# Kernel tuning notes

Hardware: AMD Instinct MI355X
Metric: run time of the kernel (lower is better)

Reference implementation:

```python
import jax, jax.numpy as jnp
from jax import lax
import numpy as np

EPS = 1e-3  # keras BatchNormalization default epsilon

def _bn(x, g, b, m, v):
    return (x - m) / jnp.sqrt(v + EPS) * g + b

def _conv_relu(x, w, b):
    y = lax.conv_general_dilated(x, w, (1, 1), 'SAME', dimension_numbers=('NHWC', 'HWIO', 'NHWC'))
    return jax.nn.relu(y + b)

def _pool(x):
    return lax.reduce_window(x, -jnp.inf, lax.max, (1, 2, 2, 1), (1, 2, 2, 1), 'VALID')

def setup_inputs():
    key = jax.random.key(0)
    ks = jax.random.split(key, 24)
    B, E = 2048, 16
    rn = lambda k, s, sc=0.05: jax.random.normal(k, s, jnp.float32) * sc
    pos = lambda k, s: jax.random.uniform(k, s, jnp.float32, 0.5, 1.5)
    inp = {}
    inp['x'] = jax.random.normal(ks[0], (B, 32, 32, 3), jnp.float32)
    inp['cW1'] = rn(ks[1], (3, 3, 3, 32), 0.2); inp['cb1'] = jnp.zeros((32,), jnp.float32)
    inp['bn1g'] = pos(ks[2], (32,)); inp['bn1b'] = rn(ks[3], (32,))
    inp['bn1m'] = rn(ks[4], (32,)); inp['bn1v'] = pos(ks[5], (32,))
    inp['cW2'] = rn(ks[6], (3, 3, 32, 64), 0.1); inp['cb2'] = jnp.zeros((64,), jnp.float32)
    inp['bn2g'] = pos(ks[7], (64,)); inp['bn2b'] = rn(ks[8], (64,))
    inp['bn2m'] = rn(ks[9], (64,)); inp['bn2v'] = pos(ks[10], (64,))
    inp['dW'] = rn(ks[11], (4096, 128), 0.02); inp['db'] = jnp.zeros((128,), jnp.float32)
    inp['rW1'] = rn(ks[12], (128, 64), 0.1); inp['rb1'] = jnp.zeros((64,), jnp.float32)
    inp['rW2'] = rn(ks[13], (64, E), 0.1); inp['rb2'] = jnp.zeros((E,), jnp.float32)
    inp['eW1'] = rn(ks[14], (E, 128, 128), 0.1); inp['eb1'] = jnp.zeros((E, 128), jnp.float32)
    inp['ebng'] = pos(ks[15], (E, 128)); inp['ebnb'] = rn(ks[16], (E, 128))
    inp['ebnm'] = rn(ks[17], (E, 128)); inp['ebnv'] = pos(ks[18], (E, 128))
    inp['eW2'] = rn(ks[19], (E, 128, 64), 0.1); inp['eb2'] = jnp.zeros((E, 64), jnp.float32)
    inp['eW3'] = rn(ks[20], (E, 64, 10), 0.1); inp['eb3'] = jnp.zeros((E, 10), jnp.float32)
    return inp

def reference(x, cW1, cb1, bn1g, bn1b, bn1m, bn1v, cW2, cb2, bn2g, bn2b, bn2m, bn2v,
              dW, db, rW1, rb1, rW2, rb2, eW1, eb1, ebng, ebnb, ebnm, ebnv, eW2, eb2, eW3, eb3):
    # shared trunk: conv(relu) -> BN -> maxpool, twice; flatten; dense(relu). Dropout = identity (inference).
    h = _pool(_bn(_conv_relu(x, cW1, cb1), bn1g, bn1b, bn1m, bn1v))   # [B,16,16,32]
    h = _pool(_bn(_conv_relu(h, cW2, cb2), bn2g, bn2b, bn2m, bn2v))   # [B,8,8,64]
    feats = jax.nn.relu(h.reshape(h.shape[0], -1) @ dW + db)          # [B,128]
    # router softmax over expert logits
    router_logits = jax.nn.relu(feats @ rW1 + rb1) @ rW2 + rb2        # [B,E]
    router_probs = jax.nn.softmax(router_logits, axis=-1)
    # all experts fused into batched GEMMs over stacked weights: [E,B,*]
    e = jax.nn.relu(jnp.einsum('bd,edh->ebh', feats, eW1) + eb1[:, None, :])
    e = _bn(e, ebng[:, None, :], ebnb[:, None, :], ebnm[:, None, :], ebnv[:, None, :])
    e = jax.nn.relu(jnp.einsum('ebh,ehk->ebk', e, eW2) + eb2[:, None, :])
    e = jnp.einsum('ebk,ekc->ebc', e, eW3) + eb3[:, None, :]          # [E,B,10]
    # weighted sum combine: sum_e probs[b,e] * logits[e,b,c]
    return jnp.einsum('ebc,be->bc', e, router_probs)
```

## Files before the change

### kernel.cpp

```cpp
#include <hip/hip_runtime.h>

#define EPS 1e-3f

typedef _Float16 half8 __attribute__((ext_vector_type(8)));
typedef _Float16 half4v __attribute__((ext_vector_type(4)));
typedef float f32x4 __attribute__((ext_vector_type(4)));

__global__ __launch_bounds__(256) void k_wprep_all(
    const float* __restrict__ dW,  _Float16* __restrict__ Wt2,
    const float* __restrict__ eW1, _Float16* __restrict__ eW1t,
    const float* __restrict__ eW2, _Float16* __restrict__ eW2t,
    const float* __restrict__ cW1, _Float16* __restrict__ Wt1,
    const float* __restrict__ cW2, _Float16* __restrict__ Wt,
    const float* __restrict__ eW3, _Float16* __restrict__ eW3p)
{
    __shared__ _Float16 lsbuf[16640];
    int bx = blockIdx.x, tid = threadIdx.x;

    if (bx < 64) {
        auto lt = (_Float16(*)[137])lsbuf;
        int kb = bx * 64;
        int c = tid & 127, r2 = tid >> 7;
#pragma unroll
        for (int it = 0; it < 32; ++it) {
            int r = it * 2 + r2;
            lt[r][c] = (_Float16)dW[(long)(kb + r) * 128 + c];
        }
        __syncthreads();
#pragma unroll
        for (int it = 0; it < 4; ++it) {
            int chunk = it * 256 + tid;
            int n = chunk >> 3, kc = (chunk & 7) * 8;
            half8 v;
#pragma unroll
            for (int j = 0; j < 8; ++j) v[j] = lt[kc + j][n];
            *(half8*)(Wt2 + (long)n * 4096 + kb + kc) = v;
        }
    } else if (bx < 80) {
        auto lt = (_Float16(*)[130])lsbuf;
        int e = bx - 64;
        const float* src = eW1 + (long)e * 16384;
#pragma unroll
        for (int it = 0; it < 64; ++it) {
            int idx = it * 256 + tid;
            lt[idx >> 7][idx & 127] = (_Float16)src[idx];
        }
        __syncthreads();
        _Float16* dst = eW1t + (long)e * 16384;
#pragma unroll
        for (int it = 0; it < 64; ++it) {
            int idx = it * 256 + tid;
            dst[idx] = lt[idx & 127][idx >> 7];
        }
    } else if (bx < 96) {
        auto lt = (_Float16(*)[66])lsbuf;
        int e = bx - 80;
        const float* src = eW2 + (long)e * 8192;
#pragma unroll
        for (int it = 0; it < 32; ++it) {
            int idx = it * 256 + tid;
            lt[idx >> 6][idx & 63] = (_Float16)src[idx];
        }
        __syncthreads();
        _Float16* dst = eW2t + (long)e * 8192;
#pragma unroll
        for (int it = 0; it < 32; ++it) {
            int idx = it * 256 + tid;
            dst[idx] = lt[idx & 127][idx >> 7];
        }
    } else {
        int t = (bx - 96) * 256 + tid;
        if (t < 3072) {
            int k = t & 31, co = (t >> 5) & 31, ky = t >> 10;
            int kx = k >> 2, ci = k & 3;
            float val = (kx < 3 && ci < 3) ? cW1[((ky * 3 + kx) * 3 + ci) * 32 + co] : 0.f;
            Wt1[t] = (_Float16)val;
        } else if (t < 3072 + 18432) {
            int u = t - 3072;
            int co = u & 63;
            int rest = u >> 6;
            int ci = rest & 31, tap = rest >> 5;
            Wt[(tap * 64 + co) * 32 + ci] = (_Float16)cW2[u];
        } else if (t < 3072 + 18432 + 16384) {
            int u = t - 21504;
            int k = u & 63, n = (u >> 6) & 15, e = u >> 10;
            float val = (n < 10) ? eW3[(e * 64 + k) * 10 + n] : 0.f;
            eW3p[(e * 16 + n) * 64 + k] = (_Float16)val;
        }
    }
}

__global__ __launch_bounds__(256) void k_conv1_mfma(
    const float* __restrict__ x, const _Float16* __restrict__ Wt1,
    const float* __restrict__ bias,
    const float* __restrict__ g, const float* __restrict__ bb,
    const float* __restrict__ m, const float* __restrict__ v,
    _Float16* __restrict__ out)
{
    __shared__ __align__(16) _Float16 As[34][40][4];
    int tid = threadIdx.x;
    int b = blockIdx.x;
    int w = tid >> 6, l = tid & 63;
    int l15 = l & 15, lq = l >> 4;

    {
        float4 z = make_float4(0.f, 0.f, 0.f, 0.f);
        float4* flat = (float4*)&As[0][0][0];
        for (int i = tid; i < 680; i += 256) flat[i] = z;
    }
    __syncthreads();

    {
        int y = tid >> 3, x0 = (tid & 7) * 4;
        const float* src = x + ((long)b * 1024 + y * 32 + x0) * 3;
        float4 f0 = *(const float4*)(src);
        float4 f1 = *(const float4*)(src + 4);
        float4 f2 = *(const float4*)(src + 8);
        half4v h0 = { (_Float16)f0.x, (_Float16)f0.y, (_Float16)f0.z, (_Float16)0.f };
        half4v h1 = { (_Float16)f0.w, (_Float16)f1.x, (_Float16)f1.y, (_Float16)0.f };
        half4v h2 = { (_Float16)f1.z, (_Float16)f1.w, (_Float16)f2.x, (_Float16)0.f };
        half4v h3 = { (_Float16)f2.y, (_Float16)f2.z, (_Float16)f2.w, (_Float16)0.f };
        *(half4v*)&As[y + 1][x0 + 1][0] = h0;
        *(half4v*)&As[y + 1][x0 + 2][0] = h1;
        *(half4v*)&As[y + 1][x0 + 3][0] = h2;
        *(half4v*)&As[y + 1][x0 + 4][0] = h3;
    }

    half8 bf[3][2];
#pragma unroll
    for (int ky = 0; ky < 3; ++ky)
#pragma unroll
        for (int nf = 0; nf < 2; ++nf)
            bf[ky][nf] = *(const half8*)(Wt1 + (ky * 32 + nf * 16 + l15) * 32 + lq * 8);

    float bv[2], gg[2], iv[2], mm[2], bbv[2];
#pragma unroll
    for (int nf = 0; nf < 2; ++nf) {
        int co = nf * 16 + l15;
        bv[nf] = bias[co]; gg[nf] = g[co]; bbv[nf] = bb[co]; mm[nf] = m[co];
        iv[nf] = rsqrtf(v[co] + EPS);
    }
    __syncthreads();

    int y0 = w * 8;
#pragma unroll
    for (int pr = 0; pr < 4; ++pr) {
        int ya = y0 + 2 * pr;
        f32x4 acc[2][2][2];
#pragma unroll
        for (int r = 0; r < 2; ++r)
#pragma unroll
            for (int h = 0; h < 2; ++h)
#pragma unroll
                for (int nf = 0; nf < 2; ++nf)
                    acc[r][h][nf] = (f32x4){ bv[nf], bv[nf], bv[nf], bv[nf] };

#pragma unroll
        for (int ky = 0; ky < 3; ++ky)
#pragma unroll
            for (int r = 0; r < 2; ++r)
#pragma unroll
                for (int h = 0; h < 2; ++h) {
                    const _Float16* ap = &As[ya + r + ky][h * 16 + l15 + 2 * lq][0];
                    half4v a0 = *(const half4v*)ap;
                    half4v a1 = *(const half4v*)(ap + 4);
                    half8 af = __builtin_shufflevector(a0, a1, 0, 1, 2, 3, 4, 5, 6, 7);
#pragma unroll
                    for (int nf = 0; nf < 2; ++nf)
                        acc[r][h][nf] = __builtin_amdgcn_mfma_f32_16x16x32_f16(
                            af, bf[ky][nf], acc[r][h][nf], 0, 0, 0);
                }

        int py = w * 4 + pr;
#pragma unroll
        for (int h = 0; h < 2; ++h)
#pragma unroll
            for (int nf = 0; nf < 2; ++nf) {
                f32x4 aA = acc[0][h][nf], aB = acc[1][h][nf];
                float p0 = fmaxf(fmaxf(aA[0], aA[1]), fmaxf(aB[0], aB[1]));
                float p1 = fmaxf(fmaxf(aA[2], aA[3]), fmaxf(aB[2], aB[3]));
                p0 = fmaxf(p0, 0.f); p1 = fmaxf(p1, 0.f);
                p0 = (p0 - mm[nf]) * iv[nf] * gg[nf] + bbv[nf];
                p1 = (p1 - mm[nf]) * iv[nf] * gg[nf] + bbv[nf];
                int px = h * 8 + lq * 2;
                int co = nf * 16 + l15;
                long base = (((long)b * 16 + py) * 16 + px) * 32 + co;
                out[base]      = (_Float16)p0;
                out[base + 32] = (_Float16)p1;
            }
    }
}

__global__ __launch_bounds__(256) void k_conv2_mfma(
    const _Float16* __restrict__ h1f, const _Float16* __restrict__ Wt,
    const float* __restrict__ bias,
    const float* __restrict__ g, const float* __restrict__ bb,
    const float* __restrict__ m, const float* __restrict__ v,
    _Float16* __restrict__ out)
{
    __shared__ __align__(16) _Float16 As[18][18][40];
    int tid = threadIdx.x;
    int b   = blockIdx.x;
    int w   = tid >> 6;
    int l   = tid & 63;
    int l15 = l & 15, lq = l >> 4;

    {
        _Float16* flat = &As[0][0][0];
        for (int i = tid * 8; i < 18 * 18 * 40; i += 256 * 8)
            *(float4*)(flat + i) = make_float4(0.f, 0.f, 0.f, 0.f);
    }
    __syncthreads();

    {
        const _Float16* src = h1f + ((long)b * 256 + tid) * 32;
        _Float16* dst = &As[(tid >> 4) + 1][(tid & 15) + 1][0];
#pragma unroll
        for (int i = 0; i < 4; ++i)
            *(half8*)(dst + i * 8) = *(const half8*)(src + i * 8);
    }

    f32x4 acc[4][4];
#pragma unroll
    for (int nf = 0; nf < 4; ++nf) {
        float bv = bias[nf * 16 + l15];
#pragma unroll
        for (int mf = 0; mf < 4; ++mf)
            acc[mf][nf] = (f32x4){ bv, bv, bv, bv };
    }
    __syncthreads();

    int row0 = 4 * w;
#pragma unroll
    for (int tap = 0; tap < 9; ++tap) {
        int ky = tap / 3, kx = tap % 3;
        half8 bf[4];
        const _Float16* wb = Wt + ((long)(tap * 64 + l15)) * 32 + lq * 8;
#pragma unroll
        for (int nf = 0; nf < 4; ++nf)
            bf[nf] = *(const half8*)(wb + (long)nf * 16 * 32);
#pragma unroll
        for (int mf = 0; mf < 4; ++mf) {
            const _Float16* ap = &As[row0 + mf + ky][l15 + kx][lq * 8];
            half8 af = *(const half8*)ap;
#pragma unroll
            for (int nf = 0; nf < 4; ++nf)
                acc[mf][nf] = __builtin_amdgcn_mfma_f32_16x16x32_f16(
                    af, bf[nf], acc[mf][nf], 0, 0, 0);
        }
    }

#pragma unroll
    for (int nf = 0; nf < 4; ++nf) {
        int co = nf * 16 + l15;
        float gg = g[co], bbv = bb[co], mm = m[co];
        float iv = rsqrtf(v[co] + EPS);
#pragma unroll
        for (int pr = 0; pr < 2; ++pr) {
            int prow = 2 * w + pr;
            f32x4 a0 = acc[2 * pr][nf];
            f32x4 a1 = acc[2 * pr + 1][nf];
            float p0 = fmaxf(fmaxf(a0[0], a0[1]), fmaxf(a1[0], a1[1]));
            float p1 = fmaxf(fmaxf(a0[2], a0[3]), fmaxf(a1[2], a1[3]));
            p0 = fmaxf(p0, 0.f);
            p1 = fmaxf(p1, 0.f);
            int ppx = lq * 2;
            long base = (((long)b * 8 + prow) * 8) * 64 + co;
            out[base + (long)(ppx    ) * 64] = (_Float16)((p0 - mm) * iv * gg + bbv);
            out[base + (long)(ppx + 1) * 64] = (_Float16)((p1 - mm) * iv * gg + bbv);
        }
    }
}

__global__ __launch_bounds__(256) void k_dense_mfma(
    const _Float16* __restrict__ h2f, const _Float16* __restrict__ Wt2,
    float* __restrict__ pws)
{
    __shared__ __align__(16) _Float16 As[16][264];
    int tid = threadIdx.x;
    int w = tid >> 6, l = tid & 63;
    int l15 = l & 15, lq = l >> 4;
    int brow = blockIdx.x * 16;
    int kbase = blockIdx.y * 512;
    int n0 = w * 32;

    f32x4 acc[2] = { (f32x4){0.f,0.f,0.f,0.f}, (f32x4){0.f,0.f,0.f,0.f} };

    int srow = tid >> 4, sc = (tid & 15) * 16;
#pragma unroll
    for (int k0 = 0; k0 < 512; k0 += 256) {
        __syncthreads();
        const _Float16* src = h2f + (long)(brow + srow) * 4096 + kbase + k0 + sc;
        half8 v0 = *(const half8*)src;
        half8 v1 = *(const half8*)(src + 8);
        *(half8*)(&As[srow][sc])     = v0;
        *(half8*)(&As[srow][sc + 8]) = v1;
        __syncthreads();
#pragma unroll
        for (int kk = 0; kk < 256; kk += 32) {
            half8 af = *(const half8*)(&As[l15][kk + lq * 8]);
#pragma unroll
            for (int nf = 0; nf < 2; ++nf) {
                half8 bf = *(const half8*)(Wt2 + (long)(n0 + nf * 16 + l15) * 4096
                                           + kbase + k0 + kk + lq * 8);
                acc[nf] = __builtin_amdgcn_mfma_f32_16x16x32_f16(af, bf, acc[nf], 0, 0, 0);
            }
        }
    }

    float* pbase = pws + (long)blockIdx.y * 262144;
#pragma unroll
    for (int nf = 0; nf < 2; ++nf) {
        int n = n0 + nf * 16 + l15;
#pragma unroll
        for (int reg = 0; reg < 4; ++reg) {
            int b = brow + lq * 4 + reg;
            pbase[(long)b * 128 + n] = acc[nf][reg];
        }
    }
}

__global__ __launch_bounds__(256) void k_reduce_router(
    const float* __restrict__ pws, const float* __restrict__ db,
    const float* __restrict__ rW1, const float* __restrict__ rb1,
    const float* __restrict__ rW2, const float* __restrict__ rb2,
    _Float16* __restrict__ featsH, float* __restrict__ probs)
{
    __shared__ float fsm[16][128];
    __shared__ float r1s[16][64];
    int tid = threadIdx.x;
    int brow = blockIdx.x * 16;
    int r = tid >> 4, c0 = (tid & 15) * 8;

    float acc[8];
#pragma unroll
    for (int j = 0; j < 8; ++j) acc[j] = db[c0 + j];
    long base = (long)(brow + r) * 128 + c0;
#pragma unroll
    for (int kc = 0; kc < 8; ++kc) {
        const float4* p = (const float4*)(pws + (long)kc * 262144 + base);
        float4 v0 = p[0], v1 = p[1];
        acc[0] += v0.x; acc[1] += v0.y; acc[2] += v0.z; acc[3] += v0.w;
        acc[4] += v1.x; acc[5] += v1.y; acc[6] += v1.z; acc[7] += v1.w;
    }
    half8 hv;
#pragma unroll
    for (int j = 0; j < 8; ++j) {
        float val = fmaxf(acc[j], 0.f);
        fsm[r][c0 + j] = val;
        hv[j] = (_Float16)val;
    }
    *(half8*)(featsH + base) = hv;
    __syncthreads();

    {
        int h = tid & 63, bg = tid >> 6;
        float a[4];
#pragma unroll
        for (int i = 0; i < 4; ++i) a[i] = rb1[h];
        for (int d = 0; d < 128; ++d) {
            float wgt = rW1[d * 64 + h];
#pragma unroll
            for (int i = 0; i < 4; ++i) a[i] += fsm[bg * 4 + i][d] * wgt;
        }
#pragma unroll
        for (int i = 0; i < 4; ++i) r1s[bg * 4 + i][h] = fmaxf(a[i], 0.f);
    }
    __syncthreads();

    {
        int b = tid >> 4, e = tid & 15;
        float a = rb2[e];
#pragma unroll 8
        for (int k = 0; k < 64; ++k) a += r1s[b][k] * rW2[k * 16 + e];
        float mx = a;
#pragma unroll
        for (int off = 1; off < 16; off <<= 1)
            mx = fmaxf(mx, __shfl_xor(mx, off, 16));
        float ex = __expf(a - mx);
        float s = ex;
#pragma unroll
        for (int off = 1; off < 16; off <<= 1)
            s += __shfl_xor(s, off, 16);
        probs[(long)(brow + b) * 16 + e] = ex / s;
    }
}

__global__ __launch_bounds__(256) void k_expert_mfma(
    const _Float16* __restrict__ featsH,
    const _Float16* __restrict__ eW1t, const float* __restrict__ eb1,
    const float* __restrict__ g,  const float* __restrict__ bb,
    const float* __restrict__ m,  const float* __restrict__ v,
    const _Float16* __restrict__ eW2t, const float* __restrict__ eb2,
    const _Float16* __restrict__ eW3p, const float* __restrict__ eb3,
    float* __restrict__ e3p)
{
    __shared__ __align__(16) _Float16 fsH[64][136];
    __shared__ __align__(16) _Float16 h1sH[64][136];
    __shared__ __align__(16) _Float16 h2sH[64][72];
    int e = blockIdx.x, bt = blockIdx.y;
    int tid = threadIdx.x;
    int w = tid >> 6, l = tid & 63, l15 = l & 15, lq = l >> 4;
    int brow = bt * 64, m0 = w * 16;

#pragma unroll
    for (int it = 0; it < 4; ++it) {
        int idx = it * 256 + tid;
        int r = idx >> 4, c = (idx & 15) * 8;
        *(half8*)&fsH[r][c] = *(const half8*)(featsH + (long)(brow + r) * 128 + c);
    }
    __syncthreads();

    {
        half8 af[4];
#pragma unroll
        for (int kq = 0; kq < 4; ++kq)
            af[kq] = *(const half8*)&fsH[m0 + l15][kq * 32 + lq * 8];
        const _Float16* B1 = eW1t + (long)e * 16384 + l15 * 128 + lq * 8;
        f32x4 acc[8];
#pragma unroll
        for (int nf = 0; nf < 8; ++nf) {
            float bv = eb1[e * 128 + nf * 16 + l15];
            acc[nf] = (f32x4){ bv, bv, bv, bv };
        }
#pragma unroll
        for (int nf = 0; nf < 8; ++nf)
#pragma unroll
            for (int kq = 0; kq < 4; ++kq) {
                half8 bfv = *(const half8*)(B1 + nf * 2048 + kq * 32);
                acc[nf] = __builtin_amdgcn_mfma_f32_16x16x32_f16(af[kq], bfv, acc[nf], 0, 0, 0);
            }
#pragma unroll
        for (int nf = 0; nf < 8; ++nf) {
            int h = nf * 16 + l15;
            float gg = g[e * 128 + h], bbv = bb[e * 128 + h], mm = m[e * 128 + h];
            float iv = rsqrtf(v[e * 128 + h] + EPS);
#pragma unroll
            for (int reg = 0; reg < 4; ++reg) {
                float val = fmaxf(acc[nf][reg], 0.f);
                h1sH[m0 + lq * 4 + reg][h] = (_Float16)((val - mm) * iv * gg + bbv);
            }
        }
    }
    __syncthreads();

    {
        half8 af[4];
#pragma unroll
        for (int kq = 0; kq < 4; ++kq)
            af[kq] = *(const half8*)&h1sH[m0 + l15][kq * 32 + lq * 8];
        const _Float16* B2 = eW2t + (long)e * 8192 + l15 * 128 + lq * 8;
        f32x4 acc[4];
#pragma unroll
        for (int nf = 0; nf < 4; ++nf) {
            float bv = eb2[e * 64 + nf * 16 + l15];
            acc[nf] = (f32x4){ bv, bv, bv, bv };
        }
#pragma unroll
        for (int nf = 0; nf < 4; ++nf)
#pragma unroll
            for (int kq = 0; kq < 4; ++kq) {
                half8 bfv = *(const half8*)(B2 + nf * 2048 + kq * 32);
                acc[nf] = __builtin_amdgcn_mfma_f32_16x16x32_f16(af[kq], bfv, acc[nf], 0, 0, 0);
            }
#pragma unroll
        for (int nf = 0; nf < 4; ++nf)
#pragma unroll
            for (int reg = 0; reg < 4; ++reg)
                h2sH[m0 + lq * 4 + reg][nf * 16 + l15] = (_Float16)fmaxf(acc[nf][reg], 0.f);
    }
    __syncthreads();

    {
        half8 af[2];
#pragma unroll
        for (int kq = 0; kq < 2; ++kq)
            af[kq] = *(const half8*)&h2sH[m0 + l15][kq * 32 + lq * 8];
        const _Float16* B3 = eW3p + (long)e * 1024 + l15 * 64 + lq * 8;
        float bv = (l15 < 10) ? eb3[e * 10 + l15] : 0.f;
        f32x4 acc = (f32x4){ bv, bv, bv, bv };
#pragma unroll
        for (int kq = 0; kq < 2; ++kq) {
            half8 bfv = *(const half8*)(B3 + kq * 32);
            acc = __builtin_amdgcn_mfma_f32_16x16x32_f16(af[kq], bfv, acc, 0, 0, 0);
        }
#pragma unroll
        for (int reg = 0; reg < 4; ++reg) {
            int b = brow + m0 + lq * 4 + reg;
            e3p[((long)e * 2048 + b) * 16 + l15] = acc[reg];
        }
    }
}

__global__ __launch_bounds__(256) void k_combine(
    const float* __restrict__ e3p, const float* __restrict__ probs,
    float* __restrict__ out)
{
    int t = blockIdx.x * blockDim.x + threadIdx.x;
    if (t >= 2048 * 10) return;
    int b = t / 10, c = t % 10;
    float acc = 0.f;
#pragma unroll
    for (int e = 0; e < 16; ++e)
        acc += probs[(long)b * 16 + e] * e3p[((long)e * 2048 + b) * 16 + c];
    out[t] = acc;
}

extern "C" void kernel_launch(void* const* d_in, const int* in_sizes, int n_in,
                              void* d_out, int out_size, void* d_ws, size_t ws_size,
                              hipStream_t stream)
{
    const float* x    = (const float*)d_in[0];
    const float* cW1  = (const float*)d_in[1];
    const float* cb1  = (const float*)d_in[2];
    const float* bn1g = (const float*)d_in[3];
    const float* bn1b = (const float*)d_in[4];
    const float* bn1m = (const float*)d_in[5];
    const float* bn1v = (const float*)d_in[6];
    const float* cW2  = (const float*)d_in[7];
    const float* cb2  = (const float*)d_in[8];
    const float* bn2g = (const float*)d_in[9];
    const float* bn2b = (const float*)d_in[10];
    const float* bn2m = (const float*)d_in[11];
    const float* bn2v = (const float*)d_in[12];
    const float* dW   = (const float*)d_in[13];
    const float* db   = (const float*)d_in[14];
    const float* rW1  = (const float*)d_in[15];
    const float* rb1  = (const float*)d_in[16];
    const float* rW2  = (const float*)d_in[17];
    const float* rb2  = (const float*)d_in[18];
    const float* eW1  = (const float*)d_in[19];
    const float* eb1  = (const float*)d_in[20];
    const float* ebng = (const float*)d_in[21];
    const float* ebnb = (const float*)d_in[22];
    const float* ebnm = (const float*)d_in[23];
    const float* ebnv = (const float*)d_in[24];
    const float* eW2  = (const float*)d_in[25];
    const float* eb2  = (const float*)d_in[26];
    const float* eW3  = (const float*)d_in[27];
    const float* eb3  = (const float*)d_in[28];

    float* ws    = (float*)d_ws;
    float* h1reg = ws;
    _Float16* h1f = (_Float16*)h1reg;
    float* e3p   = h1reg;
    _Float16* featsH = (_Float16*)(h1reg + 524288);
    float* h2reg = h1reg + 16777216;
    _Float16* h2f = (_Float16*)h2reg;
    _Float16* Wt2 = (_Float16*)(h2reg + 4194304);
    float* probs = h2reg + 8388608;
    float* ewreg = probs + 32768;
    _Float16* eW1t = (_Float16*)ewreg;
    _Float16* eW2t = eW1t + 262144;
    _Float16* eW3p = eW2t + 131072;
    _Float16* Wt   = eW3p + 16384;
    _Float16* Wt1  = Wt + 18432;
    float* pws   = ewreg + 262144;
    float* out   = (float*)d_out;

    k_wprep_all<<<244, 256, 0, stream>>>(dW, Wt2, eW1, eW1t, eW2, eW2t,
                                         cW1, Wt1, cW2, Wt, eW3, eW3p);
    k_conv1_mfma<<<2048, 256, 0, stream>>>(x, Wt1, cb1, bn1g, bn1b, bn1m, bn1v, h1f);
    k_conv2_mfma<<<2048, 256, 0, stream>>>(h1f, Wt, cb2, bn2g, bn2b, bn2m, bn2v, h2f);
    {
        dim3 grid(128, 8);
        k_dense_mfma<<<grid, 256, 0, stream>>>(h2f, Wt2, pws);
    }
    k_reduce_router<<<128, 256, 0, stream>>>(pws, db, rW1, rb1, rW2, rb2,
                                             featsH, probs);
    {
        dim3 grid(16, 32);
        k_expert_mfma<<<grid, 256, 0, stream>>>(featsH, eW1t, eb1, ebng, ebnb, ebnm, ebnv,
                                                eW2t, eb2, eW3p, eb3, e3p);
    }
    k_combine<<<80, 256, 0, stream>>>(e3p, probs, out);
}
```

Baseline: 104.3 us.

## Fuse conv1 and conv2 into one kernel keeping pooled activations in LDS

Merges the two conv+ReLU+BN+pool kernels into a single per-image kernel. The conv1 pooled output is written directly into the padded shared-memory tile that conv2 reads, instead of going to global memory and being reloaded. This removes the global write and read of the intermediate activation (about 32 KB fp16 per image) and one launch. In exchange the kernel uses more LDS (both tiles live at once), which may lower occupancy, and conv1's scattered 2-byte stores now go to LDS, where they may hit bank conflicts.

```diff
diff --git a/kernel.cpp b/kernel.cpp
--- a/kernel.cpp
+++ b/kernel.cpp
@@ -90,14 +90,19 @@
     }
 }
 
-__global__ __launch_bounds__(256) void k_conv1_mfma(
+__global__ __launch_bounds__(256) void k_conv12(
     const float* __restrict__ x, const _Float16* __restrict__ Wt1,
-    const float* __restrict__ bias,
-    const float* __restrict__ g, const float* __restrict__ bb,
-    const float* __restrict__ m, const float* __restrict__ v,
+    const float* __restrict__ b1, const float* __restrict__ g1,
+    const float* __restrict__ bb1, const float* __restrict__ m1,
+    const float* __restrict__ v1,
+    const _Float16* __restrict__ Wt,
+    const float* __restrict__ b2, const float* __restrict__ g2,
+    const float* __restrict__ bb2, const float* __restrict__ m2,
+    const float* __restrict__ v2,
     _Float16* __restrict__ out)
 {
-    __shared__ __align__(16) _Float16 As[34][40][4];
+    __shared__ __align__(16) _Float16 As1[34][40][4];
+    __shared__ __align__(16) _Float16 As2[18][18][40];
     int tid = threadIdx.x;
     int b = blockIdx.x;
     int w = tid >> 6, l = tid & 63;
@@ -105,8 +110,10 @@
 
     {
         float4 z = make_float4(0.f, 0.f, 0.f, 0.f);
-        float4* flat = (float4*)&As[0][0][0];
-        for (int i = tid; i < 680; i += 256) flat[i] = z;
+        float4* f1p = (float4*)&As1[0][0][0];
+        for (int i = tid; i < 680; i += 256) f1p[i] = z;
+        float4* f2p = (float4*)&As2[0][0][0];
+        for (int i = tid; i < 1620; i += 256) f2p[i] = z;
     }
     __syncthreads();
 
@@ -120,115 +127,86 @@
         half4v h1 = { (_Float16)f0.w, (_Float16)f1.x, (_Float16)f1.y, (_Float16)0.f };
         half4v h2 = { (_Float16)f1.z, (_Float16)f1.w, (_Float16)f2.x, (_Float16)0.f };
         half4v h3 = { (_Float16)f2.y, (_Float16)f2.z, (_Float16)f2.w, (_Float16)0.f };
-        *(half4v*)&As[y + 1][x0 + 1][0] = h0;
-        *(half4v*)&As[y + 1][x0 + 2][0] = h1;
-        *(half4v*)&As[y + 1][x0 + 3][0] = h2;
-        *(half4v*)&As[y + 1][x0 + 4][0] = h3;
-    }
-
-    half8 bf[3][2];
+        *(half4v*)&As1[y + 1][x0 + 1][0] = h0;
+        *(half4v*)&As1[y + 1][x0 + 2][0] = h1;
+        *(half4v*)&As1[y + 1][x0 + 3][0] = h2;
+        *(half4v*)&As1[y + 1][x0 + 4][0] = h3;
+    }
+
+    half8 bf1[3][2];
 #pragma unroll
     for (int ky = 0; ky < 3; ++ky)
 #pragma unroll
         for (int nf = 0; nf < 2; ++nf)
-            bf[ky][nf] = *(const half8*)(Wt1 + (ky * 32 + nf * 16 + l15) * 32 + lq * 8);
-
-    float bv[2], gg[2], iv[2], mm[2], bbv[2];
+            bf1[ky][nf] = *(const half8*)(Wt1 + (ky * 32 + nf * 16 + l15) * 32 + lq * 8);
+
+    float bv1[2], gg1[2], iv1[2], mm1[2], bbv1[2];
 #pragma unroll
     for (int nf = 0; nf < 2; ++nf) {
         int co = nf * 16 + l15;
-        bv[nf] = bias[co]; gg[nf] = g[co]; bbv[nf] = bb[co]; mm[nf] = m[co];
-        iv[nf] = rsqrtf(v[co] + EPS);
-    }
-    __syncthreads();
-
-    int y0 = w * 8;
-#pragma unroll
-    for (int pr = 0; pr < 4; ++pr) {
-        int ya = y0 + 2 * pr;
-        f32x4 acc[2][2][2];
-#pragma unroll
-        for (int r = 0; r < 2; ++r)
+        bv1[nf] = b1[co]; gg1[nf] = g1[co]; bbv1[nf] = bb1[co]; mm1[nf] = m1[co];
+        iv1[nf] = rsqrtf(v1[co] + EPS);
+    }
+    __syncthreads();
+
+    {
+        int y0 = w * 8;
+#pragma unroll
+        for (int pr = 0; pr < 4; ++pr) {
+            int ya = y0 + 2 * pr;
+            f32x4 acc[2][2][2];
+#pragma unroll
+            for (int r = 0; r < 2; ++r)
+#pragma unroll
+                for (int h = 0; h < 2; ++h)
+#pragma unroll
+                    for (int nf = 0; nf < 2; ++nf)
+                        acc[r][h][nf] = (f32x4){ bv1[nf], bv1[nf], bv1[nf], bv1[nf] };
+
+#pragma unroll
+            for (int ky = 0; ky < 3; ++ky)
+#pragma unroll
+                for (int r = 0; r < 2; ++r)
+#pragma unroll
+                    for (int h = 0; h < 2; ++h) {
+                        const _Float16* ap = &As1[ya + r + ky][h * 16 + l15 + 2 * lq][0];
+                        half4v a0 = *(const half4v*)ap;
+                        half4v a1 = *(const half4v*)(ap + 4);
+                        half8 af = __builtin_shufflevector(a0, a1, 0, 1, 2, 3, 4, 5, 6, 7);
+#pragma unroll
+                        for (int nf = 0; nf < 2; ++nf)
+                            acc[r][h][nf] = __builtin_amdgcn_mfma_f32_16x16x32_f16(
+                                af, bf1[ky][nf], acc[r][h][nf], 0, 0, 0);
+                    }
+
+            int py = w * 4 + pr;
 #pragma unroll
             for (int h = 0; h < 2; ++h)
 #pragma unroll
-                for (int nf = 0; nf < 2; ++nf)
-                    acc[r][h][nf] = (f32x4){ bv[nf], bv[nf], bv[nf], bv[nf] };
-
-#pragma unroll
-        for (int ky = 0; ky < 3; ++ky)
-#pragma unroll
-            for (int r = 0; r < 2; ++r)
-#pragma unroll
-                for (int h = 0; h < 2; ++h) {
-                    const _Float16* ap = &As[ya + r + ky][h * 16 + l15 + 2 * lq][0];
-                    half4v a0 = *(const half4v*)ap;
-                    half4v a1 = *(const half4v*)(ap + 4);
-                    half8 af = __builtin_shufflevector(a0, a1, 0, 1, 2, 3, 4, 5, 6, 7);
-#pragma unroll
-                    for (int nf = 0; nf < 2; ++nf)
-                        acc[r][h][nf] = __builtin_amdgcn_mfma_f32_16x16x32_f16(
-                            af, bf[ky][nf], acc[r][h][nf], 0, 0, 0);
+                for (int nf = 0; nf < 2; ++nf) {
+                    f32x4 aA = acc[0][h][nf], aB = acc[1][h][nf];
+                    float p0 = fmaxf(fmaxf(aA[0], aA[1]), fmaxf(aB[0], aB[1]));
+                    float p1 = fmaxf(fmaxf(aA[2], aA[3]), fmaxf(aB[2], aB[3]));
+                    p0 = fmaxf(p0, 0.f); p1 = fmaxf(p1, 0.f);
+                    p0 = (p0 - mm1[nf]) * iv1[nf] * gg1[nf] + bbv1[nf];
+                    p1 = (p1 - mm1[nf]) * iv1[nf] * gg1[nf] + bbv1[nf];
+                    int px = h * 8 + lq * 2;
+                    int co = nf * 16 + l15;
+                    As2[py + 1][px + 1][co] = (_Float16)p0;
+                    As2[py + 1][px + 2][co] = (_Float16)p1;
                 }
-
-        int py = w * 4 + pr;
-#pragma unroll
-        for (int h = 0; h < 2; ++h)
-#pragma unroll
-            for (int nf = 0; nf < 2; ++nf) {
-                f32x4 aA = acc[0][h][nf], aB = acc[1][h][nf];
-                float p0 = fmaxf(fmaxf(aA[0], aA[1]), fmaxf(aB[0], aB[1]));
-                float p1 = fmaxf(fmaxf(aA[2], aA[3]), fmaxf(aB[2], aB[3]));
-                p0 = fmaxf(p0, 0.f); p1 = fmaxf(p1, 0.f);
-                p0 = (p0 - mm[nf]) * iv[nf] * gg[nf] + bbv[nf];
-                p1 = (p1 - mm[nf]) * iv[nf] * gg[nf] + bbv[nf];
-                int px = h * 8 + lq * 2;
-                int co = nf * 16 + l15;
-                long base = (((long)b * 16 + py) * 16 + px) * 32 + co;
-                out[base]      = (_Float16)p0;
-                out[base + 32] = (_Float16)p1;
-            }
-    }
-}
-
-__global__ __launch_bounds__(256) void k_conv2_mfma(
-    const _Float16* __restrict__ h1f, const _Float16* __restrict__ Wt,
-    const float* __restrict__ bias,
-    const float* __restrict__ g, const float* __restrict__ bb,
-    const float* __restrict__ m, const float* __restrict__ v,
-    _Float16* __restrict__ out)
-{
-    __shared__ __align__(16) _Float16 As[18][18][40];
-    int tid = threadIdx.x;
-    int b   = blockIdx.x;
-    int w   = tid >> 6;
-    int l   = tid & 63;
-    int l15 = l & 15, lq = l >> 4;
-
-    {
-        _Float16* flat = &As[0][0][0];
-        for (int i = tid * 8; i < 18 * 18 * 40; i += 256 * 8)
-            *(float4*)(flat + i) = make_float4(0.f, 0.f, 0.f, 0.f);
-    }
-    __syncthreads();
-
-    {
-        const _Float16* src = h1f + ((long)b * 256 + tid) * 32;
-        _Float16* dst = &As[(tid >> 4) + 1][(tid & 15) + 1][0];
-#pragma unroll
-        for (int i = 0; i < 4; ++i)
-            *(half8*)(dst + i * 8) = *(const half8*)(src + i * 8);
-    }
-
-    f32x4 acc[4][4];
+        }
+    }
+    __syncthreads();
+
+    f32x4 acc2[4][4];
 #pragma unroll
     for (int nf = 0; nf < 4; ++nf) {
-        float bv = bias[nf * 16 + l15];
+        float bv = b2[nf * 16 + l15];
 #pragma unroll
         for (int mf = 0; mf < 4; ++mf)
-            acc[mf][nf] = (f32x4){ bv, bv, bv, bv };
-    }
-    __syncthreads();
+            acc2[mf][nf] = (f32x4){ bv, bv, bv, bv };
+    }
 
     int row0 = 4 * w;
 #pragma unroll
@@ -241,25 +219,25 @@
             bf[nf] = *(const half8*)(wb + (long)nf * 16 * 32);
 #pragma unroll
         for (int mf = 0; mf < 4; ++mf) {
-            const _Float16* ap = &As[row0 + mf + ky][l15 + kx][lq * 8];
+            const _Float16* ap = &As2[row0 + mf + ky][l15 + kx][lq * 8];
             half8 af = *(const half8*)ap;
 #pragma unroll
             for (int nf = 0; nf < 4; ++nf)
-                acc[mf][nf] = __builtin_amdgcn_mfma_f32_16x16x32_f16(
-                    af, bf[nf], acc[mf][nf], 0, 0, 0);
+                acc2[mf][nf] = __builtin_amdgcn_mfma_f32_16x16x32_f16(
+                    af, bf[nf], acc2[mf][nf], 0, 0, 0);
         }
     }
 
 #pragma unroll
     for (int nf = 0; nf < 4; ++nf) {
         int co = nf * 16 + l15;
-        float gg = g[co], bbv = bb[co], mm = m[co];
-        float iv = rsqrtf(v[co] + EPS);
+        float gg = g2[co], bbv = bb2[co], mm = m2[co];
+        float iv = rsqrtf(v2[co] + EPS);
 #pragma unroll
         for (int pr = 0; pr < 2; ++pr) {
             int prow = 2 * w + pr;
-            f32x4 a0 = acc[2 * pr][nf];
-            f32x4 a1 = acc[2 * pr + 1][nf];
+            f32x4 a0 = acc2[2 * pr][nf];
+            f32x4 a1 = acc2[2 * pr + 1][nf];
             float p0 = fmaxf(fmaxf(a0[0], a0[1]), fmaxf(a1[0], a1[1]));
             float p1 = fmaxf(fmaxf(a0[2], a0[3]), fmaxf(a1[2], a1[3]));
             p0 = fmaxf(p0, 0.f);
@@ -542,7 +520,6 @@
 
     float* ws    = (float*)d_ws;
     float* h1reg = ws;
-    _Float16* h1f = (_Float16*)h1reg;
     float* e3p   = h1reg;
     _Float16* featsH = (_Float16*)(h1reg + 524288);
     float* h2reg = h1reg + 16777216;
@@ -560,8 +537,8 @@
 
     k_wprep_all<<<244, 256, 0, stream>>>(dW, Wt2, eW1, eW1t, eW2, eW2t,
                                          cW1, Wt1, cW2, Wt, eW3, eW3p);
-    k_conv1_mfma<<<2048, 256, 0, stream>>>(x, Wt1, cb1, bn1g, bn1b, bn1m, bn1v, h1f);
-    k_conv2_mfma<<<2048, 256, 0, stream>>>(h1f, Wt, cb2, bn2g, bn2b, bn2m, bn2v, h2f);
+    k_conv12<<<2048, 256, 0, stream>>>(x, Wt1, cb1, bn1g, bn1b, bn1m, bn1v,
+                                       Wt, cb2, bn2g, bn2b, bn2m, bn2v, h2f);
     {
         dim3 grid(128, 8);
         k_dense_mfma<<<grid, 256, 0, stream>>>(h2f, Wt2, pws);
```

After: 88.10 us. 15.5% less time.
